# Kernel optimization log

Hardware: AMD Instinct MI355X
Metric: run time of the kernel (lower is better)

## Reference

```python
import jax, jax.numpy as jnp
import numpy as np

B, T, I = 64, 512, 128
H, R, DA, C = 256, 20, 50, 10

def setup_inputs() -> dict:
    key = jax.random.key(0)
    ks = jax.random.split(key, 8)
    s = 0.05
    return {
        "x": jax.random.normal(ks[0], (B, T, I), dtype=jnp.float32),
        "W_ih": jax.random.normal(ks[1], (I, 4 * H), dtype=jnp.float32) * s,
        "W_hh": jax.random.normal(ks[2], (H, 4 * H), dtype=jnp.float32) * s,
        "b": jnp.zeros((4 * H,), dtype=jnp.float32),
        "W1": jax.random.normal(ks[3], (DA, I), dtype=jnp.float32) * s,
        "b1": jnp.zeros((DA,), dtype=jnp.float32),
        "W2": jax.random.normal(ks[4], (R, DA), dtype=jnp.float32) * s,
        "b2": jnp.zeros((R,), dtype=jnp.float32),
        "Wfc": jax.random.normal(ks[5], (C, H), dtype=jnp.float32) * s,
        "bfc": jnp.zeros((C,), dtype=jnp.float32),
    }

def reference(x, W_ih, W_hh, b, W1, b1, W2, b2, Wfc, bfc):
    # Dropout is identity (eval mode). Attention scores for all timesteps at once.
    bsz, seq, inp = x.shape
    hid = W_hh.shape[0]
    r = W2.shape[0]
    # scores: [B, T, r]
    S = jnp.tanh(jnp.einsum('bti,di->btd', x, W1) + b1)
    S = jnp.einsum('btd,rd->btr', S, W2) + b2
    # Prefix softmax over time via cumulative sums (softmax shift-invariant,
    # use global max over time per (b, r) for stability).
    E = jnp.exp(S - jnp.max(S, axis=1, keepdims=True))          # [B, T, r]
    denom = jnp.cumsum(E, axis=1)                               # [B, T, r]
    numer = jnp.cumsum(E[:, :, :, None] * x[:, :, None, :], axis=1)  # [B, T, r, I]
    M = jnp.mean(numer / denom[:, :, :, None], axis=2)          # [B, T, I]
    # Precompute input contribution to gates for all steps.
    gx = jnp.einsum('bti,ig->btg', M, W_ih) + b                 # [B, T, 4H]
    h0 = jnp.ones((bsz, hid), dtype=x.dtype)
    c0 = jnp.ones((bsz, hid), dtype=x.dtype)

    def step(carry, g_x):
        h, c = carry
        g = g_x + h @ W_hh
        i_t = jax.nn.sigmoid(g[:, :hid])
        f_t = jax.nn.sigmoid(g[:, hid:2 * hid])
        g_t = jnp.tanh(g[:, 2 * hid:3 * hid])
        o_t = jax.nn.sigmoid(g[:, 3 * hid:])
        c = f_t * c + i_t * g_t
        h = o_t * jnp.tanh(c)
        return (h, c), None

    (h_T, _), _ = jax.lax.scan(step, (h0, c0), jnp.swapaxes(gx, 0, 1))
    logits = h_T @ Wfc.T + bfc                                  # [B, C]
    return jax.nn.softmax(logits, axis=1)
```

## Files before the change

kernel.cpp:

```cpp
#include <hip/hip_runtime.h>
#include <hip/hip_fp16.h>

#define B_   64
#define T_   512
#define I_   128
#define H_   256
#define G4_  1024
#define R_   20
#define DA_  50
#define C_   10

typedef _Float16 half2_t __attribute__((ext_vector_type(2)));
typedef _Float16 half8_t __attribute__((ext_vector_type(8)));

__device__ __forceinline__ float fsigmoid(float x) {
  return __fdividef(1.0f, 1.0f + __expf(-x));
}
__device__ __forceinline__ float ftanh(float x) {
  return 1.0f - __fdividef(2.0f, __expf(2.0f * x) + 1.0f);
}

__global__ __launch_bounds__(256) void k0_pack(const float* __restrict__ Whh,
                                               half2_t* __restrict__ Wq) {
  int idx = blockIdx.x * 256 + threadIdx.x;
  int g = idx & 1023, k2 = idx >> 10;
  half2_t h;
  h.x = (_Float16)Whh[(2 * k2) * G4_ + g];
  h.y = (_Float16)Whh[(2 * k2 + 1) * G4_ + g];
  Wq[g * 128 + k2] = h;
}

__global__ __launch_bounds__(256) void k_init(unsigned long long* __restrict__ Hx) {
  int i = blockIdx.x * 256 + threadIdx.x;
  Hx[i] = 0ull;
}

__global__ __launch_bounds__(256) void k1_scores(const float* __restrict__ x,
                                                 const float* __restrict__ W1,
                                                 const float* __restrict__ b1,
                                                 const float* __restrict__ W2,
                                                 const float* __restrict__ b2,
                                                 float* __restrict__ S) {
  __shared__ float xs[64][129];
  __shared__ float w1s[128][64];
  __shared__ float a1s[64][53];
  int blk = blockIdx.x;
  int tid = threadIdx.x;
  int row0 = blk * 64;
  const float4* xv = (const float4*)(x + (size_t)row0 * I_);
#pragma unroll
  for (int ch = 0; ch < 8; ch++) {
    int fidx = ch * 256 + tid;
    int r = fidx >> 5, k4 = (fidx & 31) << 2;
    float4 f = xv[fidx];
    xs[r][k4] = f.x; xs[r][k4 + 1] = f.y; xs[r][k4 + 2] = f.z; xs[r][k4 + 3] = f.w;
  }
  const float4* w1v = (const float4*)W1;
#pragma unroll
  for (int ch = 0; ch < 7; ch++) {
    int fidx = ch * 256 + tid;
    if (fidx < 1600) {
      int d = fidx >> 5, k4 = (fidx & 31) << 2;
      float4 f = w1v[fidx];
      w1s[k4][d] = f.x; w1s[k4 + 1][d] = f.y; w1s[k4 + 2][d] = f.z; w1s[k4 + 3][d] = f.w;
    }
  }
  __syncthreads();
  int ty = tid >> 4, tx = tid & 15;
  float acc[4][4] = {};
#pragma unroll 4
  for (int k = 0; k < I_; k++) {
    float a0 = xs[4 * ty][k], a1 = xs[4 * ty + 1][k];
    float a2 = xs[4 * ty + 2][k], a3 = xs[4 * ty + 3][k];
    float4 bq = *(const float4*)&w1s[k][tx << 2];
    acc[0][0] += a0 * bq.x; acc[0][1] += a0 * bq.y; acc[0][2] += a0 * bq.z; acc[0][3] += a0 * bq.w;
    acc[1][0] += a1 * bq.x; acc[1][1] += a1 * bq.y; acc[1][2] += a1 * bq.z; acc[1][3] += a1 * bq.w;
    acc[2][0] += a2 * bq.x; acc[2][1] += a2 * bq.y; acc[2][2] += a2 * bq.z; acc[2][3] += a2 * bq.w;
    acc[3][0] += a3 * bq.x; acc[3][1] += a3 * bq.y; acc[3][2] += a3 * bq.z; acc[3][3] += a3 * bq.w;
  }
#pragma unroll
  for (int i = 0; i < 4; i++) {
#pragma unroll
    for (int j = 0; j < 4; j++) {
      int col = (tx << 2) + j;
      if (col < DA_) a1s[4 * ty + i][col] = tanhf(acc[i][j] + b1[col]);
    }
  }
  __syncthreads();
  int row = tid & 63, rq = tid >> 6;
  int bt = row0 + row;
  int b = bt >> 9, t = bt & 511;
#pragma unroll
  for (int m = 0; m < 5; m++) {
    int r = rq + (m << 2);
    float acc2 = b2[r];
#pragma unroll 10
    for (int d = 0; d < DA_; d++) acc2 += a1s[row][d] * W2[r * DA_ + d];
    S[((size_t)(b * R_ + r)) * T_ + t] = acc2;
  }
}

__global__ __launch_bounds__(64) void k2_prefix(const float* __restrict__ S,
                                                float* __restrict__ E,
                                                float* __restrict__ invd) {
  int br = blockIdx.x;
  int l = threadIdx.x;
  const float* Sr = S + (size_t)br * T_;
  float v[8];
  float m = -1e30f;
#pragma unroll
  for (int c = 0; c < 8; c++) {
    v[c] = Sr[c * 64 + l];
    m = fmaxf(m, v[c]);
  }
#pragma unroll
  for (int off = 32; off; off >>= 1) m = fmaxf(m, __shfl_xor(m, off));
  float carry = 0.f;
  for (int c = 0; c < 8; c++) {
    float e = expf(v[c] - m);
    float s = e;
#pragma unroll
    for (int off = 1; off < 64; off <<= 1) {
      float u = __shfl_up(s, off);
      if (l >= off) s += u;
    }
    E[(size_t)br * T_ + c * 64 + l] = e;
    invd[(size_t)br * T_ + c * 64 + l] = 1.f / (carry + s);
    carry += __shfl(s, 63);
  }
}

__global__ __launch_bounds__(128) void k3a(const float* __restrict__ x,
                                           const float* __restrict__ E,
                                           float* __restrict__ P) {
  int b = blockIdx.x >> 3, c = blockIdx.x & 7;
  int i = threadIdx.x;
  int t0 = c * 64;
  __shared__ float es[2][R_];
  float acc[R_];
#pragma unroll
  for (int r = 0; r < R_; r++) acc[r] = 0.f;
  float rE = 0.f;
  if (i < R_) rE = E[((size_t)(b * R_ + i)) * T_ + t0];
  const float* xb = x + (size_t)b * T_ * I_;
  float xv = xb[(size_t)t0 * I_ + i];
  int buf = 0;
  for (int tt = 0; tt < 64; tt++) {
    if (i < R_) es[buf][i] = rE;
    __syncthreads();
    if (tt + 1 < 64) {
      if (i < R_) rE = E[((size_t)(b * R_ + i)) * T_ + t0 + tt + 1];
    }
    float xcur = xv;
    if (tt + 1 < 64) xv = xb[(size_t)(t0 + tt + 1) * I_ + i];
#pragma unroll
    for (int r = 0; r < R_; r++) acc[r] += es[buf][r] * xcur;
    buf ^= 1;
  }
#pragma unroll
  for (int r = 0; r < R_; r++)
    P[(size_t)((b * 8 + c) * R_ + r) * I_ + i] = acc[r];
}

__global__ __launch_bounds__(256) void k3b(float* __restrict__ P) {
  int gid = blockIdx.x * 256 + threadIdx.x;
  int i = gid & 127;
  int r = (gid >> 7) % R_;
  int b = gid / (R_ * I_);
  float s = 0.f;
#pragma unroll
  for (int c = 0; c < 8; c++) {
    size_t idx = (size_t)((b * 8 + c) * R_ + r) * I_ + i;
    float v = P[idx];
    P[idx] = s;
    s += v;
  }
}

__global__ __launch_bounds__(128) void k3c(const float* __restrict__ x,
                                           const float* __restrict__ E,
                                           const float* __restrict__ invd,
                                           const float* __restrict__ P,
                                           float* __restrict__ M) {
  int b = blockIdx.x >> 3, c = blockIdx.x & 7;
  int i = threadIdx.x;
  int t0 = c * 64;
  __shared__ float es[2][R_], ds[2][R_];
  float acc[R_];
#pragma unroll
  for (int r = 0; r < R_; r++)
    acc[r] = P[(size_t)((b * 8 + c) * R_ + r) * I_ + i];
  float rE = 0.f, rD = 0.f;
  if (i < R_)
    rE = E[((size_t)(b * R_ + i)) * T_ + t0];
  else if (i < 2 * R_)
    rD = invd[((size_t)(b * R_ + (i - R_))) * T_ + t0];
  const float* xb = x + (size_t)b * T_ * I_;
  float xv = xb[(size_t)t0 * I_ + i];
  int buf = 0;
  for (int tt = 0; tt < 64; tt++) {
    if (i < R_) es[buf][i] = rE;
    else if (i < 2 * R_) ds[buf][i - R_] = rD;
    __syncthreads();
    if (tt + 1 < 64) {
      if (i < R_)
        rE = E[((size_t)(b * R_ + i)) * T_ + t0 + tt + 1];
      else if (i < 2 * R_)
        rD = invd[((size_t)(b * R_ + (i - R_))) * T_ + t0 + tt + 1];
    }
    float xcur = xv;
    if (tt + 1 < 64) xv = xb[(size_t)(t0 + tt + 1) * I_ + i];
    float s = 0.f;
#pragma unroll
    for (int r = 0; r < R_; r++) {
      acc[r] += es[buf][r] * xcur;
      s += acc[r] * ds[buf][r];
    }
    M[(size_t)b * T_ * I_ + (size_t)(t0 + tt) * I_ + i] = s * (1.0f / R_);
    buf ^= 1;
  }
}

__global__ __launch_bounds__(256) void k4_gemm(const float* __restrict__ Mm,
                                               const float* __restrict__ Wih,
                                               const float* __restrict__ bg,
                                               __half* __restrict__ gx) {
  __shared__ float As[I_][64];
  __shared__ float Bs[I_][64];
  int row0 = blockIdx.x * 64, col0 = blockIdx.y * 64;
  int tid = threadIdx.x;
#pragma unroll
  for (int ch = 0; ch < 8; ch++) {
    int fidx = ch * 256 + tid;
    int r = fidx >> 5;
    int kk = (fidx & 31) << 2;
    float4 f = ((const float4*)(Mm + (size_t)(row0 + r) * I_))[fidx & 31];
    As[kk + 0][r] = f.x;
    As[kk + 1][r] = f.y;
    As[kk + 2][r] = f.z;
    As[kk + 3][r] = f.w;
  }
#pragma unroll
  for (int ch = 0; ch < 8; ch++) {
    int fidx = ch * 256 + tid;
    int k = fidx >> 4;
    int c4 = (fidx & 15) << 2;
    float4 f = *((const float4*)(Wih + (size_t)k * G4_ + col0 + c4));
    *((float4*)&Bs[k][c4]) = f;
  }
  __syncthreads();
  int ty = tid >> 4, tx = tid & 15;
  float acc[4][4] = {};
#pragma unroll 4
  for (int k = 0; k < I_; k++) {
    float4 a = *((float4*)&As[k][ty << 2]);
    float4 bq = *((float4*)&Bs[k][tx << 2]);
    acc[0][0] += a.x * bq.x; acc[0][1] += a.x * bq.y; acc[0][2] += a.x * bq.z; acc[0][3] += a.x * bq.w;
    acc[1][0] += a.y * bq.x; acc[1][1] += a.y * bq.y; acc[1][2] += a.y * bq.z; acc[1][3] += a.y * bq.w;
    acc[2][0] += a.z * bq.x; acc[2][1] += a.z * bq.y; acc[2][2] += a.z * bq.z; acc[2][3] += a.z * bq.w;
    acc[3][0] += a.w * bq.x; acc[3][1] += a.w * bq.y; acc[3][2] += a.w * bq.z; acc[3][3] += a.w * bq.w;
  }
#pragma unroll
  for (int ii = 0; ii < 4; ii++) {
#pragma unroll
    for (int jj = 0; jj < 4; jj++) {
      int row = row0 + (ty << 2) + ii;
      int col = col0 + (tx << 2) + jj;
      gx[(size_t)row * G4_ + col] = __float2half(acc[ii][jj] + bg[col]);
    }
  }
}

union WREG {
  unsigned u[64];
  half2_t h[64];
  uint4 q[16];
};

__global__ __launch_bounds__(512, 2) void k5_lstm(
    const __half* __restrict__ gx, const half2_t* __restrict__ Wq,
    unsigned long long* __restrict__ Hx, float* __restrict__ hT) {
  int b = blockIdx.x & 63;
  int p = blockIdx.x >> 6;
  int tid = threadIdx.x;
  int wave = tid >> 6;
  int lane = tid & 63;
  int kh = lane & 1;
  int gate = (lane >> 1) & 3;
  int uw = lane >> 3;
  int u = wave * 8 + uw;
  int gcol = gate * H_ + p * 64 + u;

  __shared__ __align__(16) unsigned hsU[2][128];

  int qi = tid >> 5;
  int q_ = qi + (qi >= p ? 1 : 0);
  int d_ = tid & 31;

  WREG w;
  {
    const uint4* wp = (const uint4*)(Wq + (size_t)gcol * 128 + kh * 64);
#pragma unroll
    for (int i = 0; i < 16; i++) w.q[i] = wp[i];
  }
#pragma unroll
  for (int j = 0; j < 64; j++) asm volatile("" : "+v"(w.u[j]));

  float cstate = 1.0f;
  const __half* gxb = gx + (size_t)b * T_ * G4_;

  for (int t = 0; t < T_; t++) {
    float gxv = 0.f;
    if (!kh) gxv = (float)gxb[(size_t)t * G4_ + gcol];

    if (t == 0) {
      if (tid < 128) hsU[0][tid] = 0x3C003C00u;
    } else if (tid < 96) {
      const unsigned long long* src =
          Hx + ((size_t)(t & 1) * 64 + b) * 128 + q_ * 32 + d_;
      unsigned long long v;
      do {
        v = __hip_atomic_load(src, __ATOMIC_RELAXED, __HIP_MEMORY_SCOPE_AGENT);
      } while ((unsigned)(v >> 32) != (unsigned)t);
      hsU[t & 1][q_ * 32 + d_] = (unsigned)v;
    }
    __syncthreads();

    const half2_t* hb = (const half2_t*)hsU[t & 1] + kh * 64;
    float a0 = 0.f, a1 = 0.f, a2 = 0.f, a3 = 0.f;
#pragma unroll
    for (int i = 0; i < 16; i++) {
      half8_t hv = *(const half8_t*)(hb + i * 4);
      half2_t h0 = ((half2_t*)&hv)[0], h1 = ((half2_t*)&hv)[1];
      half2_t h2 = ((half2_t*)&hv)[2], h3 = ((half2_t*)&hv)[3];
      a0 = __builtin_amdgcn_fdot2(w.h[4 * i + 0], h0, a0, false);
      a1 = __builtin_amdgcn_fdot2(w.h[4 * i + 1], h1, a1, false);
      a2 = __builtin_amdgcn_fdot2(w.h[4 * i + 2], h2, a2, false);
      a3 = __builtin_amdgcn_fdot2(w.h[4 * i + 3], h3, a3, false);
    }
    float s = (a0 + a1) + (a2 + a3);
    s += __shfl_xor(s, 1);
    s += gxv;

    float f1 = __shfl_down(s, 2);
    float f2 = __shfl_down(s, 4);
    float f3 = __shfl_down(s, 6);
    unsigned hu = 0;
    if ((lane & 7) == 0) {
      float vi = fsigmoid(s);
      float vf = fsigmoid(f1);
      float vg = ftanh(f2);
      float vo = fsigmoid(f3);
      cstate = vf * cstate + vi * vg;
      float h = vo * ftanh(cstate);
      hu = (unsigned)__half_as_ushort(__float2half(h));
      if (t == T_ - 1) hT[b * H_ + p * 64 + u] = h;
    }
    unsigned hup = (unsigned)__shfl_down((int)hu, 8);
    if ((lane & 15) == 0 && (t + 1) < T_) {
      unsigned h2pack = hu | (hup << 16);
      int slot = p * 32 + wave * 4 + (lane >> 4);
      unsigned long long pkt =
          (unsigned long long)h2pack |
          ((unsigned long long)(unsigned)(t + 1) << 32);
      unsigned long long* dst =
          Hx + ((size_t)((t + 1) & 1) * 64 + b) * 128 + slot;
      __hip_atomic_store(dst, pkt, __ATOMIC_RELAXED, __HIP_MEMORY_SCOPE_AGENT);
      hsU[(t + 1) & 1][slot] = h2pack;
    }
  }
}

__global__ __launch_bounds__(64) void k6_head(const float* __restrict__ hT,
                                              const float* __restrict__ Wfc,
                                              const float* __restrict__ bfc,
                                              float* __restrict__ out) {
  int b = blockIdx.x, l = threadIdx.x;
  const float* h = hT + b * H_;
  float p[C_];
#pragma unroll
  for (int c = 0; c < C_; c++) p[c] = 0.f;
#pragma unroll
  for (int q = 0; q < 4; q++) {
    float hv = h[q * 64 + l];
#pragma unroll
    for (int c = 0; c < C_; c++) p[c] += hv * Wfc[c * H_ + q * 64 + l];
  }
#pragma unroll
  for (int c = 0; c < C_; c++)
    for (int off = 32; off; off >>= 1) p[c] += __shfl_xor(p[c], off);
  if (l == 0) {
    float m = -1e30f, e[C_], sum = 0.f;
    for (int c = 0; c < C_; c++) { p[c] += bfc[c]; m = fmaxf(m, p[c]); }
    for (int c = 0; c < C_; c++) { e[c] = expf(p[c] - m); sum += e[c]; }
    for (int c = 0; c < C_; c++) out[b * C_ + c] = e[c] / sum;
  }
}

extern "C" void kernel_launch(void* const* d_in, const int* in_sizes, int n_in,
                              void* d_out, int out_size, void* d_ws, size_t ws_size,
                              hipStream_t stream) {
  const float* x   = (const float*)d_in[0];
  const float* Wih = (const float*)d_in[1];
  const float* Whh = (const float*)d_in[2];
  const float* bg  = (const float*)d_in[3];
  const float* W1  = (const float*)d_in[4];
  const float* b1  = (const float*)d_in[5];
  const float* W2  = (const float*)d_in[6];
  const float* b2  = (const float*)d_in[7];
  const float* Wfc = (const float*)d_in[8];
  const float* bfc = (const float*)d_in[9];
  float* out = (float*)d_out;

  float* wsf = (float*)d_ws;
  unsigned long long* Hx = (unsigned long long*)wsf;
  float* S    = wsf;
  float* E    = wsf + 655360;
  float* INVD = wsf + 1310720;
  float* Mm   = wsf + 1966080;
  float* hT   = wsf + 6160384;
  half2_t* Wq = (half2_t*)(wsf + 6176768);
  __half* gx  = (__half*)(wsf + 6307840);
  float* P    = wsf + 6307840;

  hipLaunchKernelGGL(k0_pack,   dim3(512),     dim3(256), 0, stream, Whh, Wq);
  hipLaunchKernelGGL(k1_scores, dim3(512),     dim3(256), 0, stream, x, W1, b1, W2, b2, S);
  hipLaunchKernelGGL(k2_prefix, dim3(B_ * R_), dim3(64),  0, stream, S, E, INVD);
  hipLaunchKernelGGL(k3a,       dim3(512),     dim3(128), 0, stream, x, E, P);
  hipLaunchKernelGGL(k3b,       dim3(640),     dim3(256), 0, stream, P);
  hipLaunchKernelGGL(k3c,       dim3(512),     dim3(128), 0, stream, x, E, INVD, P, Mm);
  hipLaunchKernelGGL(k4_gemm,   dim3(512, 16), dim3(256), 0, stream, Mm, Wih, bg, gx);
  hipLaunchKernelGGL(k_init,    dim3(64),      dim3(256), 0, stream, Hx);
  hipLaunchKernelGGL(k5_lstm,   dim3(256),     dim3(512), 0, stream, gx, Wq, Hx, hT);
  hipLaunchKernelGGL(k6_head,   dim3(B_),      dim3(64),  0, stream, hT, Wfc, bfc, out);
}
```

Baseline: 1.140 ms.

## Run each batch LSTM in a single 1024-thread block, dropping cross-block exchange

The recurrent LSTM kernel now runs one 1024-thread workgroup per batch element instead of four cooperating workgroups that exchanged hidden-state slices through global-memory atomics with spin-waiting. Each thread computes one full gate dot product over all 256 hidden inputs. It keeps 228 weights in registers and spills the remaining 28 weights per thread into LDS, so the recurrence needs only a workgroup barrier per step. In exchange, only 64 workgroups occupy the GPU, each thread does twice the serial dot-product work, and register pressure is high with a risk of spills.

Measured after the change: 1.628 ms. 42.7% more time.

```diff
diff --git a/kernel.cpp b/kernel.cpp
--- a/kernel.cpp
+++ b/kernel.cpp
@@ -10,6 +10,9 @@
 #define DA_  50
 #define C_   10
 
+#define NV_  114
+#define NL_  14
+
 typedef _Float16 half2_t __attribute__((ext_vector_type(2)));
 typedef _Float16 half8_t __attribute__((ext_vector_type(8)));
 
@@ -18,6 +21,9 @@
 }
 __device__ __forceinline__ float ftanh(float x) {
   return 1.0f - __fdividef(2.0f, __expf(2.0f * x) + 1.0f);
+}
+__device__ __forceinline__ half2_t uh(unsigned x) {
+  union { unsigned u; half2_t h; } c; c.u = x; return c.h;
 }
 
 __global__ __launch_bounds__(256) void k0_pack(const float* __restrict__ Whh,
@@ -28,11 +34,6 @@
   h.x = (_Float16)Whh[(2 * k2) * G4_ + g];
   h.y = (_Float16)Whh[(2 * k2 + 1) * G4_ + g];
   Wq[g * 128 + k2] = h;
-}
-
-__global__ __launch_bounds__(256) void k_init(unsigned long long* __restrict__ Hx) {
-  int i = blockIdx.x * 256 + threadIdx.x;
-  Hx[i] = 0ull;
 }
 
 __global__ __launch_bounds__(256) void k1_scores(const float* __restrict__ x,
@@ -271,102 +272,102 @@
   }
 }
 
-union WREG {
-  unsigned u[64];
-  half2_t h[64];
-  uint4 q[16];
+union WREG5 {
+  unsigned u[NV_];
+  half2_t h[NV_];
+  uint4 q[NV_ / 4];
 };
 
-__global__ __launch_bounds__(512, 2) void k5_lstm(
+__global__ __launch_bounds__(1024, 4) void k5_lstm(
     const __half* __restrict__ gx, const half2_t* __restrict__ Wq,
-    unsigned long long* __restrict__ Hx, float* __restrict__ hT) {
-  int b = blockIdx.x & 63;
-  int p = blockIdx.x >> 6;
+    float* __restrict__ hT) {
+  int b = blockIdx.x;
   int tid = threadIdx.x;
-  int wave = tid >> 6;
-  int lane = tid & 63;
-  int kh = lane & 1;
-  int gate = (lane >> 1) & 3;
-  int uw = lane >> 3;
-  int u = wave * 8 + uw;
-  int gcol = gate * H_ + p * 64 + u;
+  int unit = tid >> 2, gate = tid & 3;
+  int gcol = gate * 256 + unit;
 
   __shared__ __align__(16) unsigned hsU[2][128];
-
-  int qi = tid >> 5;
-  int q_ = qi + (qi >= p ? 1 : 0);
-  int d_ = tid & 31;
-
-  WREG w;
+  __shared__ __align__(8) unsigned wlds[1024 * NL_];
+
+  WREG5 w;
   {
-    const uint4* wp = (const uint4*)(Wq + (size_t)gcol * 128 + kh * 64);
-#pragma unroll
-    for (int i = 0; i < 16; i++) w.q[i] = wp[i];
-  }
-#pragma unroll
-  for (int j = 0; j < 64; j++) asm volatile("" : "+v"(w.u[j]));
+    const uint4* wp = (const uint4*)(Wq + (size_t)gcol * 128);
+#pragma unroll
+    for (int i = 0; i < NV_ / 4; i++) w.q[i] = wp[i];
+    uint2 tl = *(const uint2*)(Wq + (size_t)gcol * 128 + 112);
+    w.u[112] = tl.x; w.u[113] = tl.y;
+  }
+#pragma unroll
+  for (int j = 0; j < NV_; j++) asm volatile("" : "+v"(w.u[j]));
+
+  {
+    const uint2* wt = (const uint2*)(Wq + (size_t)gcol * 128 + NV_);
+#pragma unroll
+    for (int i = 0; i < NL_ / 2; i++)
+      *(uint2*)&wlds[tid * NL_ + i * 2] = wt[i];
+  }
+  if (tid < 128) hsU[0][tid] = 0x3C003C00u;
 
   float cstate = 1.0f;
-  const __half* gxb = gx + (size_t)b * T_ * G4_;
+  const __half* gp = gx + (size_t)b * T_ * G4_ + gcol;
 
   for (int t = 0; t < T_; t++) {
-    float gxv = 0.f;
-    if (!kh) gxv = (float)gxb[(size_t)t * G4_ + gcol];
-
-    if (t == 0) {
-      if (tid < 128) hsU[0][tid] = 0x3C003C00u;
-    } else if (tid < 96) {
-      const unsigned long long* src =
-          Hx + ((size_t)(t & 1) * 64 + b) * 128 + q_ * 32 + d_;
-      unsigned long long v;
-      do {
-        v = __hip_atomic_load(src, __ATOMIC_RELAXED, __HIP_MEMORY_SCOPE_AGENT);
-      } while ((unsigned)(v >> 32) != (unsigned)t);
-      hsU[t & 1][q_ * 32 + d_] = (unsigned)v;
-    }
     __syncthreads();
-
-    const half2_t* hb = (const half2_t*)hsU[t & 1] + kh * 64;
+    float gxv = (float)*gp;
+    gp += G4_;
+    const half2_t* hb = (const half2_t*)hsU[t & 1];
+
     float a0 = 0.f, a1 = 0.f, a2 = 0.f, a3 = 0.f;
 #pragma unroll
-    for (int i = 0; i < 16; i++) {
+    for (int i = 0; i < 28; i++) {
       half8_t hv = *(const half8_t*)(hb + i * 4);
-      half2_t h0 = ((half2_t*)&hv)[0], h1 = ((half2_t*)&hv)[1];
-      half2_t h2 = ((half2_t*)&hv)[2], h3 = ((half2_t*)&hv)[3];
-      a0 = __builtin_amdgcn_fdot2(w.h[4 * i + 0], h0, a0, false);
-      a1 = __builtin_amdgcn_fdot2(w.h[4 * i + 1], h1, a1, false);
-      a2 = __builtin_amdgcn_fdot2(w.h[4 * i + 2], h2, a2, false);
-      a3 = __builtin_amdgcn_fdot2(w.h[4 * i + 3], h3, a3, false);
-    }
-    float s = (a0 + a1) + (a2 + a3);
-    s += __shfl_xor(s, 1);
-    s += gxv;
-
-    float f1 = __shfl_down(s, 2);
-    float f2 = __shfl_down(s, 4);
-    float f3 = __shfl_down(s, 6);
-    unsigned hu = 0;
-    if ((lane & 7) == 0) {
+      a0 = __builtin_amdgcn_fdot2(w.h[4 * i + 0], ((half2_t*)&hv)[0], a0, false);
+      a1 = __builtin_amdgcn_fdot2(w.h[4 * i + 1], ((half2_t*)&hv)[1], a1, false);
+      a2 = __builtin_amdgcn_fdot2(w.h[4 * i + 2], ((half2_t*)&hv)[2], a2, false);
+      a3 = __builtin_amdgcn_fdot2(w.h[4 * i + 3], ((half2_t*)&hv)[3], a3, false);
+    }
+    {
+      unsigned wl[NL_];
+#pragma unroll
+      for (int i = 0; i < NL_ / 2; i++) {
+        uint2 v = *(const uint2*)&wlds[tid * NL_ + i * 2];
+        wl[2 * i] = v.x; wl[2 * i + 1] = v.y;
+      }
+      half8_t hv0 = *(const half8_t*)(hb + 112);
+      half8_t hv1 = *(const half8_t*)(hb + 116);
+      half8_t hv2 = *(const half8_t*)(hb + 120);
+      half8_t hv3 = *(const half8_t*)(hb + 124);
+      a0 = __builtin_amdgcn_fdot2(w.h[112], ((half2_t*)&hv0)[0], a0, false);
+      a1 = __builtin_amdgcn_fdot2(w.h[113], ((half2_t*)&hv0)[1], a1, false);
+      a2 = __builtin_amdgcn_fdot2(uh(wl[0]), ((half2_t*)&hv0)[2], a2, false);
+      a3 = __builtin_amdgcn_fdot2(uh(wl[1]), ((half2_t*)&hv0)[3], a3, false);
+      a0 = __builtin_amdgcn_fdot2(uh(wl[2]), ((half2_t*)&hv1)[0], a0, false);
+      a1 = __builtin_amdgcn_fdot2(uh(wl[3]), ((half2_t*)&hv1)[1], a1, false);
+      a2 = __builtin_amdgcn_fdot2(uh(wl[4]), ((half2_t*)&hv1)[2], a2, false);
+      a3 = __builtin_amdgcn_fdot2(uh(wl[5]), ((half2_t*)&hv1)[3], a3, false);
+      a0 = __builtin_amdgcn_fdot2(uh(wl[6]), ((half2_t*)&hv2)[0], a0, false);
+      a1 = __builtin_amdgcn_fdot2(uh(wl[7]), ((half2_t*)&hv2)[1], a1, false);
+      a2 = __builtin_amdgcn_fdot2(uh(wl[8]), ((half2_t*)&hv2)[2], a2, false);
+      a3 = __builtin_amdgcn_fdot2(uh(wl[9]), ((half2_t*)&hv2)[3], a3, false);
+      a0 = __builtin_amdgcn_fdot2(uh(wl[10]), ((half2_t*)&hv3)[0], a0, false);
+      a1 = __builtin_amdgcn_fdot2(uh(wl[11]), ((half2_t*)&hv3)[1], a1, false);
+      a2 = __builtin_amdgcn_fdot2(uh(wl[12]), ((half2_t*)&hv3)[2], a2, false);
+      a3 = __builtin_amdgcn_fdot2(uh(wl[13]), ((half2_t*)&hv3)[3], a3, false);
+    }
+    float s = ((a0 + a1) + (a2 + a3)) + gxv;
+
+    float s1 = __shfl_down(s, 1);
+    float s2 = __shfl_down(s, 2);
+    float s3 = __shfl_down(s, 3);
+    if ((tid & 3) == 0) {
       float vi = fsigmoid(s);
-      float vf = fsigmoid(f1);
-      float vg = ftanh(f2);
-      float vo = fsigmoid(f3);
+      float vf = fsigmoid(s1);
+      float vg = ftanh(s2);
+      float vo = fsigmoid(s3);
       cstate = vf * cstate + vi * vg;
       float h = vo * ftanh(cstate);
-      hu = (unsigned)__half_as_ushort(__float2half(h));
-      if (t == T_ - 1) hT[b * H_ + p * 64 + u] = h;
-    }
-    unsigned hup = (unsigned)__shfl_down((int)hu, 8);
-    if ((lane & 15) == 0 && (t + 1) < T_) {
-      unsigned h2pack = hu | (hup << 16);
-      int slot = p * 32 + wave * 4 + (lane >> 4);
-      unsigned long long pkt =
-          (unsigned long long)h2pack |
-          ((unsigned long long)(unsigned)(t + 1) << 32);
-      unsigned long long* dst =
-          Hx + ((size_t)((t + 1) & 1) * 64 + b) * 128 + slot;
-      __hip_atomic_store(dst, pkt, __ATOMIC_RELAXED, __HIP_MEMORY_SCOPE_AGENT);
-      hsU[(t + 1) & 1][slot] = h2pack;
+      ((__half*)hsU[(t + 1) & 1])[unit] = __float2half(h);
+      if (t == T_ - 1) hT[b * H_ + unit] = h;
     }
   }
 }
@@ -413,7 +414,6 @@
   float* out = (float*)d_out;
 
   float* wsf = (float*)d_ws;
-  unsigned long long* Hx = (unsigned long long*)wsf;
   float* S    = wsf;
   float* E    = wsf + 655360;
   float* INVD = wsf + 1310720;
@@ -423,14 +423,13 @@
   __half* gx  = (__half*)(wsf + 6307840);
   float* P    = wsf + 6307840;
 
-  hipLaunchKernelGGL(k0_pack,   dim3(512),     dim3(256), 0, stream, Whh, Wq);
-  hipLaunchKernelGGL(k1_scores, dim3(512),     dim3(256), 0, stream, x, W1, b1, W2, b2, S);
-  hipLaunchKernelGGL(k2_prefix, dim3(B_ * R_), dim3(64),  0, stream, S, E, INVD);
-  hipLaunchKernelGGL(k3a,       dim3(512),     dim3(128), 0, stream, x, E, P);
-  hipLaunchKernelGGL(k3b,       dim3(640),     dim3(256), 0, stream, P);
-  hipLaunchKernelGGL(k3c,       dim3(512),     dim3(128), 0, stream, x, E, INVD, P, Mm);
-  hipLaunchKernelGGL(k4_gemm,   dim3(512, 16), dim3(256), 0, stream, Mm, Wih, bg, gx);
-  hipLaunchKernelGGL(k_init,    dim3(64),      dim3(256), 0, stream, Hx);
-  hipLaunchKernelGGL(k5_lstm,   dim3(256),     dim3(512), 0, stream, gx, Wq, Hx, hT);
-  hipLaunchKernelGGL(k6_head,   dim3(B_),      dim3(64),  0, stream, hT, Wfc, bfc, out);
-}
+  hipLaunchKernelGGL(k0_pack,   dim3(512),     dim3(256),  0, stream, Whh, Wq);
+  hipLaunchKernelGGL(k1_scores, dim3(512),     dim3(256),  0, stream, x, W1, b1, W2, b2, S);
+  hipLaunchKernelGGL(k2_prefix, dim3(B_ * R_), dim3(64),   0, stream, S, E, INVD);
+  hipLaunchKernelGGL(k3a,       dim3(512),     dim3(128),  0, stream, x, E, P);
+  hipLaunchKernelGGL(k3b,       dim3(640),     dim3(256),  0, stream, P);
+  hipLaunchKernelGGL(k3c,       dim3(512),     dim3(128),  0, stream, x, E, INVD, P, Mm);
+  hipLaunchKernelGGL(k4_gemm,   dim3(512, 16), dim3(256),  0, stream, Mm, Wih, bg, gx);
+  hipLaunchKernelGGL(k5_lstm,   dim3(B_),      dim3(1024), 0, stream, gx, Wq, hT);
+  hipLaunchKernelGGL(k6_head,   dim3(B_),      dim3(64),   0, stream, hT, Wfc, bfc, out);
+}
```

## Split LSTM recurrence across 8 blocks per batch with LDS-resident weights

Applied to the files above, without the earlier changes.

The recurrent LSTM kernel now splits each batch row's hidden units across 8 blocks of 256 threads instead of 4 blocks of 512. W_hh slices are repacked and staged in LDS, then reloaded into registers every step instead of held persistently in registers. Gate sums go through a shared array and an extra barrier, and gx columns are permuted to match. This trades more cross-block h exchange, LDS traffic and an extra sync per step for more parallel blocks and lower register pressure.

New measurement: 1.252 ms. 1.1x slower.

```diff
diff --git a/kernel.cpp b/kernel.cpp
--- a/kernel.cpp
+++ b/kernel.cpp
@@ -13,6 +13,8 @@
 typedef _Float16 half2_t __attribute__((ext_vector_type(2)));
 typedef _Float16 half8_t __attribute__((ext_vector_type(8)));
 
+union U4H { uint4 q; half2_t h[4]; };
+
 __device__ __forceinline__ float fsigmoid(float x) {
   return __fdividef(1.0f, 1.0f + __expf(-x));
 }
@@ -28,6 +30,17 @@
   h.x = (_Float16)Whh[(2 * k2) * G4_ + g];
   h.y = (_Float16)Whh[(2 * k2 + 1) * G4_ + g];
   Wq[g * 128 + k2] = h;
+}
+
+__global__ __launch_bounds__(256) void k0b_pack(const half2_t* __restrict__ Wq,
+                                                uint4* __restrict__ WP8) {
+  int j = blockIdx.x * 256 + threadIdx.x;
+  int tid = j & 255, pi = j >> 8;
+  int p = pi >> 4, i = pi & 15;
+  int c = tid >> 1, kh = tid & 1;
+  int gate = c >> 5, uloc = c & 31;
+  int gcol = gate * 256 + p * 32 + uloc;
+  WP8[j] = *(const uint4*)(Wq + (size_t)gcol * 128 + kh * 64 + 4 * i);
 }
 
 __global__ __launch_bounds__(256) void k_init(unsigned long long* __restrict__ Hx) {
@@ -266,63 +279,53 @@
     for (int jj = 0; jj < 4; jj++) {
       int row = row0 + (ty << 2) + ii;
       int col = col0 + (tx << 2) + jj;
-      gx[(size_t)row * G4_ + col] = __float2half(acc[ii][jj] + bg[col]);
-    }
-  }
-}
-
-union WREG {
-  unsigned u[64];
-  half2_t h[64];
-  uint4 q[16];
-};
-
-__global__ __launch_bounds__(512, 2) void k5_lstm(
-    const __half* __restrict__ gx, const half2_t* __restrict__ Wq,
+      int u = col & 255, g = col >> 8;
+      int perm = (u << 2) | g;
+      gx[(size_t)row * G4_ + perm] = __float2half(acc[ii][jj] + bg[col]);
+    }
+  }
+}
+
+__global__ __launch_bounds__(256, 2) void k5_lstm(
+    const __half* __restrict__ gx, const uint4* __restrict__ WP8,
     unsigned long long* __restrict__ Hx, float* __restrict__ hT) {
-  int b = blockIdx.x & 63;
-  int p = blockIdx.x >> 6;
+  int blk = blockIdx.x;
+  int b = blk & 63, p = blk >> 6;
   int tid = threadIdx.x;
-  int wave = tid >> 6;
-  int lane = tid & 63;
-  int kh = lane & 1;
-  int gate = (lane >> 1) & 3;
-  int uw = lane >> 3;
-  int u = wave * 8 + uw;
-  int gcol = gate * H_ + p * 64 + u;
-
+  int c = tid >> 1, kh = tid & 1;
+
+  __shared__ __align__(16) uint4 wlds[16 * 256];
   __shared__ __align__(16) unsigned hsU[2][128];
-
-  int qi = tid >> 5;
-  int q_ = qi + (qi >= p ? 1 : 0);
-  int d_ = tid & 31;
-
-  WREG w;
+  __shared__ float gsum[128];
+
   {
-    const uint4* wp = (const uint4*)(Wq + (size_t)gcol * 128 + kh * 64);
-#pragma unroll
-    for (int i = 0; i < 16; i++) w.q[i] = wp[i];
-  }
-#pragma unroll
-  for (int j = 0; j < 64; j++) asm volatile("" : "+v"(w.u[j]));
+    const uint4* wp = WP8 + (size_t)p * 4096;
+#pragma unroll
+    for (int i = 0; i < 16; i++) wlds[i * 256 + tid] = wp[i * 256 + tid];
+  }
+  if (tid < 128) hsU[0][tid] = 0x3C003C00u;
+  __syncthreads();
 
   float cstate = 1.0f;
-  const __half* gxb = gx + (size_t)b * T_ * G4_;
+  const __half* gxp = gx + (size_t)b * T_ * G4_ + p * 128;
+  int gxi = ((c & 31) << 2) | (c >> 5);
+  int s = (tid < p * 16) ? tid : tid + 16;
 
   for (int t = 0; t < T_; t++) {
+    uint4 w[16];
+#pragma unroll
+    for (int i = 0; i < 16; i++) w[i] = wlds[i * 256 + tid];
     float gxv = 0.f;
-    if (!kh) gxv = (float)gxb[(size_t)t * G4_ + gcol];
-
-    if (t == 0) {
-      if (tid < 128) hsU[0][tid] = 0x3C003C00u;
-    } else if (tid < 96) {
+    if (!kh) gxv = (float)gxp[(size_t)t * G4_ + gxi];
+
+    if (t > 0 && tid < 112) {
       const unsigned long long* src =
-          Hx + ((size_t)(t & 1) * 64 + b) * 128 + q_ * 32 + d_;
+          Hx + ((size_t)(t & 1) * 64 + b) * 128 + s;
       unsigned long long v;
       do {
         v = __hip_atomic_load(src, __ATOMIC_RELAXED, __HIP_MEMORY_SCOPE_AGENT);
       } while ((unsigned)(v >> 32) != (unsigned)t);
-      hsU[t & 1][q_ * 32 + d_] = (unsigned)v;
+      hsU[t & 1][s] = (unsigned)v;
     }
     __syncthreads();
 
@@ -330,43 +333,43 @@
     float a0 = 0.f, a1 = 0.f, a2 = 0.f, a3 = 0.f;
 #pragma unroll
     for (int i = 0; i < 16; i++) {
+      U4H wc; wc.q = w[i];
       half8_t hv = *(const half8_t*)(hb + i * 4);
-      half2_t h0 = ((half2_t*)&hv)[0], h1 = ((half2_t*)&hv)[1];
-      half2_t h2 = ((half2_t*)&hv)[2], h3 = ((half2_t*)&hv)[3];
-      a0 = __builtin_amdgcn_fdot2(w.h[4 * i + 0], h0, a0, false);
-      a1 = __builtin_amdgcn_fdot2(w.h[4 * i + 1], h1, a1, false);
-      a2 = __builtin_amdgcn_fdot2(w.h[4 * i + 2], h2, a2, false);
-      a3 = __builtin_amdgcn_fdot2(w.h[4 * i + 3], h3, a3, false);
-    }
-    float s = (a0 + a1) + (a2 + a3);
-    s += __shfl_xor(s, 1);
-    s += gxv;
-
-    float f1 = __shfl_down(s, 2);
-    float f2 = __shfl_down(s, 4);
-    float f3 = __shfl_down(s, 6);
-    unsigned hu = 0;
-    if ((lane & 7) == 0) {
-      float vi = fsigmoid(s);
-      float vf = fsigmoid(f1);
-      float vg = ftanh(f2);
-      float vo = fsigmoid(f3);
+      a0 = __builtin_amdgcn_fdot2(wc.h[0], ((half2_t*)&hv)[0], a0, false);
+      a1 = __builtin_amdgcn_fdot2(wc.h[1], ((half2_t*)&hv)[1], a1, false);
+      a2 = __builtin_amdgcn_fdot2(wc.h[2], ((half2_t*)&hv)[2], a2, false);
+      a3 = __builtin_amdgcn_fdot2(wc.h[3], ((half2_t*)&hv)[3], a3, false);
+    }
+    float sv = (a0 + a1) + (a2 + a3);
+    sv += __shfl_xor(sv, 1);
+    if (!kh) gsum[c] = sv + gxv;
+    __syncthreads();
+
+    if (tid < 32) {
+      float vi = gsum[tid], vf = gsum[32 + tid], vg = gsum[64 + tid],
+            vo = gsum[96 + tid];
+      vi = fsigmoid(vi);
+      vf = fsigmoid(vf);
+      vg = ftanh(vg);
+      vo = fsigmoid(vo);
       cstate = vf * cstate + vi * vg;
       float h = vo * ftanh(cstate);
-      hu = (unsigned)__half_as_ushort(__float2half(h));
-      if (t == T_ - 1) hT[b * H_ + p * 64 + u] = h;
-    }
-    unsigned hup = (unsigned)__shfl_down((int)hu, 8);
-    if ((lane & 15) == 0 && (t + 1) < T_) {
-      unsigned h2pack = hu | (hup << 16);
-      int slot = p * 32 + wave * 4 + (lane >> 4);
-      unsigned long long pkt =
-          (unsigned long long)h2pack |
-          ((unsigned long long)(unsigned)(t + 1) << 32);
-      unsigned long long* dst =
-          Hx + ((size_t)((t + 1) & 1) * 64 + b) * 128 + slot;
-      __hip_atomic_store(dst, pkt, __ATOMIC_RELAXED, __HIP_MEMORY_SCOPE_AGENT);
-      hsU[(t + 1) & 1][slot] = h2pack;
+      unsigned hu = (unsigned)__half_as_ushort(__float2half(h));
+      unsigned hup = (unsigned)__shfl_down((int)hu, 1);
+      if (!(tid & 1)) {
+        unsigned pair = hu | (hup << 16);
+        int slot = p * 16 + (tid >> 1);
+        hsU[(t + 1) & 1][slot] = pair;
+        if (t + 1 < T_) {
+          unsigned long long pkt =
+              (unsigned long long)pair |
+              ((unsigned long long)(unsigned)(t + 1) << 32);
+          __hip_atomic_store(
+              Hx + ((size_t)((t + 1) & 1) * 64 + b) * 128 + slot, pkt,
+              __ATOMIC_RELAXED, __HIP_MEMORY_SCOPE_AGENT);
+        }
+      }
+      if (t == T_ - 1) hT[b * H_ + p * 32 + tid] = h;
     }
   }
 }
@@ -413,8 +416,9 @@
   float* out = (float*)d_out;
 
   float* wsf = (float*)d_ws;
-  unsigned long long* Hx = (unsigned long long*)wsf;
   float* S    = wsf;
+  uint4* WP8  = (uint4*)wsf;
+  unsigned long long* Hx = (unsigned long long*)(wsf + 131072);
   float* E    = wsf + 655360;
   float* INVD = wsf + 1310720;
   float* Mm   = wsf + 1966080;
@@ -426,11 +430,12 @@
   hipLaunchKernelGGL(k0_pack,   dim3(512),     dim3(256), 0, stream, Whh, Wq);
   hipLaunchKernelGGL(k1_scores, dim3(512),     dim3(256), 0, stream, x, W1, b1, W2, b2, S);
   hipLaunchKernelGGL(k2_prefix, dim3(B_ * R_), dim3(64),  0, stream, S, E, INVD);
+  hipLaunchKernelGGL(k0b_pack,  dim3(128),     dim3(256), 0, stream, Wq, WP8);
+  hipLaunchKernelGGL(k_init,    dim3(64),      dim3(256), 0, stream, Hx);
   hipLaunchKernelGGL(k3a,       dim3(512),     dim3(128), 0, stream, x, E, P);
   hipLaunchKernelGGL(k3b,       dim3(640),     dim3(256), 0, stream, P);
   hipLaunchKernelGGL(k3c,       dim3(512),     dim3(128), 0, stream, x, E, INVD, P, Mm);
   hipLaunchKernelGGL(k4_gemm,   dim3(512, 16), dim3(256), 0, stream, Mm, Wih, bg, gx);
-  hipLaunchKernelGGL(k_init,    dim3(64),      dim3(256), 0, stream, Hx);
-  hipLaunchKernelGGL(k5_lstm,   dim3(256),     dim3(512), 0, stream, gx, Wq, Hx, hT);
+  hipLaunchKernelGGL(k5_lstm,   dim3(512),     dim3(256), 0, stream, gx, WP8, Hx, hT);
   hipLaunchKernelGGL(k6_head,   dim3(B_),      dim3(64),  0, stream, hT, Wfc, bfc, out);
 }
```
